# Performance work log

Hardware: AMD Instinct MI355X
Metric: run time of the kernel (lower is better)

## Reference

```python
import jax, jax.numpy as jnp
import numpy as np

N_NODES = 100000
D = 128            # node feature dim == hidden_units[0]
N_EDGES = 640000
BN_EPS = 1e-3      # keras BatchNormalization default epsilon


def setup_inputs() -> dict:
    key = jax.random.key(0)
    ks = jax.random.split(key, 12)
    node_repr = jax.random.normal(ks[0], (N_NODES, D), dtype=jnp.float32)
    edges = jax.random.randint(ks[1], (2, N_EDGES), 0, N_NODES, dtype=jnp.int64)
    # ffn_prepare: BN(D) -> Dense(D, gelu)   (dropout inactive at inference)
    bn1_gamma = jax.random.normal(ks[2], (D,), dtype=jnp.float32) * 0.1 + 1.0
    bn1_beta = jax.random.normal(ks[3], (D,), dtype=jnp.float32) * 0.1
    bn1_mean = jax.random.normal(ks[4], (D,), dtype=jnp.float32) * 0.1
    bn1_var = jax.random.uniform(ks[5], (D,), dtype=jnp.float32) + 0.5
    W1 = jax.random.normal(ks[6], (D, D), dtype=jnp.float32) / np.sqrt(D)
    b1 = jnp.zeros((D,), dtype=jnp.float32)
    # update_fn: BN(2D) -> Dense(D, gelu)
    bn2_gamma = jax.random.normal(ks[7], (2 * D,), dtype=jnp.float32) * 0.1 + 1.0
    bn2_beta = jax.random.normal(ks[8], (2 * D,), dtype=jnp.float32) * 0.1
    bn2_mean = jax.random.normal(ks[9], (2 * D,), dtype=jnp.float32) * 0.1
    bn2_var = jax.random.uniform(ks[10], (2 * D,), dtype=jnp.float32) + 0.5
    W2 = jax.random.normal(ks[11], (2 * D, D), dtype=jnp.float32) / np.sqrt(2 * D)
    b2 = jnp.zeros((D,), dtype=jnp.float32)
    return dict(node_repr=node_repr, edges=edges,
                bn1_gamma=bn1_gamma, bn1_beta=bn1_beta, bn1_mean=bn1_mean, bn1_var=bn1_var,
                W1=W1, b1=b1,
                bn2_gamma=bn2_gamma, bn2_beta=bn2_beta, bn2_mean=bn2_mean, bn2_var=bn2_var,
                W2=W2, b2=b2)


def _bn(x, gamma, beta, mean, var):
    # inference-mode batch norm
    return (x - mean) * jax.lax.rsqrt(var + BN_EPS) * gamma + beta


def reference(node_repr, edges, bn1_gamma, bn1_beta, bn1_mean, bn1_var, W1, b1,
              bn2_gamma, bn2_beta, bn2_mean, bn2_var, W2, b2):
    num_nodes = node_repr.shape[0]
    node_indices, neighbour_indices = edges[0], edges[1]
    # gather neighbour features: [E, D]
    neigh = node_repr[neighbour_indices]
    # prepare FFN (BN -> dropout(identity at eval) -> Dense + exact gelu)
    msg = jax.nn.gelu(_bn(neigh, bn1_gamma, bn1_beta, bn1_mean, bn1_var) @ W1 + b1,
                      approximate=False)
    # unsorted_segment_mean: sum / count, empty segments -> 0 (TF semantics)
    sums = jax.ops.segment_sum(msg, node_indices, num_segments=num_nodes)
    cnt = jax.ops.segment_sum(jnp.ones((edges.shape[1],), msg.dtype), node_indices,
                              num_segments=num_nodes)
    agg = sums / jnp.maximum(cnt, 1.0)[:, None]
    # update FFN on concat [node_repr, agg]: [N, 2D] -> [N, D]
    h = jnp.concatenate([node_repr, agg], axis=1)
    out = jax.nn.gelu(_bn(h, bn2_gamma, bn2_beta, bn2_mean, bn2_var) @ W2 + b2,
                      approximate=False)
    return out
```

## Files before the change

### kernel.cpp

```cpp
#include <hip/hip_runtime.h>

#define NN 100000
#define DD 128
#define EE 640000
#define BN_EPS 1e-3f
#define NBLK 391
#define NTILE 6250
#define EPB 1637
#define FFN1_BLKS 1563
#define FFN2_BLKS 768
#define LEMAX 4096

typedef __bf16 bf16x8 __attribute__((ext_vector_type(8)));
typedef float f32x4 __attribute__((ext_vector_type(4)));

#define W1F_OFF 0u
#define W2F_OFF 32768u
#define B1F_OFF 98304u
#define B2F_OFF 98816u
#define T_OFF   99328u
#define CNTG_OFF 25699328u
#define BOFS_OFF (25699328u + 611524u)
#define BSUM_OFF 26922376u
#define AGG_OFF  26926476u
#define AGG_OFF2 26926592u
#define XB_OFF   52526592u
#define PAIR_OFF 78126592u

__device__ __forceinline__ float gelu_fast(float x) {
    float x3 = x * x * x;
    float z2 = 1.5957691216057308f * x + 0.07135481627002407f * x3;
    return x / (1.0f + __expf(-z2));
}

__global__ __launch_bounds__(256) void prep_kernel(
    const float* __restrict__ g1, const float* __restrict__ be1,
    const float* __restrict__ m1, const float* __restrict__ v1,
    const float* __restrict__ W1, const float* __restrict__ b1,
    const float* __restrict__ g2, const float* __restrict__ be2,
    const float* __restrict__ m2, const float* __restrict__ v2,
    const float* __restrict__ W2, const float* __restrict__ b2,
    const int* __restrict__ edges,
    __bf16* __restrict__ W1f, __bf16* __restrict__ W2f,
    float* __restrict__ b1f, float* __restrict__ b2f,
    int* __restrict__ cntg)
{
    const int blk = blockIdx.x;
    const int t = threadIdx.x;
    if (blk < 64) {
        const int w = (blk * 256 + t) >> 6;
        const int lane = t & 63;
        if (w < 128) {
            float acc = 0.f;
            for (int k = lane; k < 128; k += 64) {
                float s = g1[k] * rsqrtf(v1[k] + BN_EPS);
                float sh = be1[k] - m1[k] * s;
                acc += sh * W1[k * 128 + w];
            }
#pragma unroll
            for (int off = 32; off > 0; off >>= 1) acc += __shfl_down(acc, off);
            if (lane == 0) b1f[w] = acc + b1[w];
        } else {
            const int n = w - 128;
            float acc = 0.f;
            for (int k = lane; k < 256; k += 64) {
                float s = g2[k] * rsqrtf(v2[k] + BN_EPS);
                float sh = be2[k] - m2[k] * s;
                acc += sh * W2[k * 128 + n];
            }
#pragma unroll
            for (int off = 32; off > 0; off >>= 1) acc += __shfl_down(acc, off);
            if (lane == 0) b2f[n] = acc + b2[n];
        }
    } else if (blk < 256) {
        int tid = (blk - 64) * 256 + t;
        if (tid < 16384) {
            int idx = tid;
            int i = idx & 7, l = (idx >> 3) & 63, nt = (idx >> 9) & 7, kt = idx >> 12;
            int k = kt * 32 + (l >> 4) * 8 + i;
            int n = nt * 16 + (l & 15);
            float s = g1[k] * rsqrtf(v1[k] + BN_EPS);
            W1f[idx] = (__bf16)(s * W1[k * 128 + n]);
        } else {
            int idx = tid - 16384;
            int i = idx & 7, l = (idx >> 3) & 63, nt = (idx >> 9) & 7, kt = idx >> 12;
            int n = nt * 16 + (l & 15);
            int row;
            if (kt < 4) {
                row = kt * 32 + (l >> 4) * 8 + i;
            } else {
                int q = (kt - 4) * 32 + (l >> 4) * 8 + i;
                row = 128 + ((q & 7) * 16 + (q >> 3));
            }
            float s = g2[row] * rsqrtf(v2[row] + BN_EPS);
            W2f[idx] = (__bf16)(s * W2[row * 128 + n]);
        }
    } else {
        __shared__ int cnt[NBLK];
        const int k = blk - 256;
        for (int b = t; b < NBLK; b += 256) cnt[b] = 0;
        __syncthreads();
        const int e0 = k * EPB, e1 = min(e0 + EPB, EE);
        for (int e = e0 + t; e < e1; e += 256)
            atomicAdd(&cnt[edges[e] >> 8], 1);
        __syncthreads();
        for (int b = t; b < NBLK; b += 256) cntg[k * NBLK + b] = cnt[b];
    }
}

__global__ __launch_bounds__(256) void sortb_kernel(const int* __restrict__ cntg,
                                                    int* __restrict__ bofs,
                                                    int* __restrict__ bsum)
{
    const int b = blockIdx.x, t = threadIdx.x;
    __shared__ int sp[256];
    int ia = 2 * t, ib = 2 * t + 1;
    int va = (ia < NBLK) ? cntg[ia * NBLK + b] : 0;
    int vb = (ib < NBLK) ? cntg[ib * NBLK + b] : 0;
    sp[t] = va + vb;
    __syncthreads();
    for (int off = 1; off < 256; off <<= 1) {
        int tmp = (t >= off) ? sp[t - off] : 0;
        __syncthreads();
        sp[t] += tmp;
        __syncthreads();
    }
    int pexcl = sp[t] - (va + vb);
    if (ia < NBLK) bofs[b * NBLK + ia] = pexcl;
    if (ib < NBLK) bofs[b * NBLK + ib] = pexcl + va;
    if (t == 255) bsum[b] = sp[255];
}

__global__ __launch_bounds__(256) void sortc_ffn1_kernel(
    const int* __restrict__ edges, const int* __restrict__ bsum,
    const int* __restrict__ bofs, int* __restrict__ pairbuf,
    const float* __restrict__ X, const __bf16* __restrict__ W1f,
    const float* __restrict__ b1f, __bf16* __restrict__ T,
    __bf16* __restrict__ Xb)
{
    __shared__ int sp[256];
    __shared__ int cur[NBLK];
    const int t = threadIdx.x;
    if (blockIdx.x < NBLK) {
        const int k = blockIdx.x;
        int ia = 2 * t, ib = 2 * t + 1;
        int va = (ia < NBLK) ? bsum[ia] : 0;
        int vb = (ib < NBLK) ? bsum[ib] : 0;
        sp[t] = va + vb;
        __syncthreads();
        for (int off = 1; off < 256; off <<= 1) {
            int tmp = (t >= off) ? sp[t - off] : 0;
            __syncthreads();
            sp[t] += tmp;
            __syncthreads();
        }
        int pexcl = sp[t] - (va + vb);
        if (ia < NBLK) cur[ia] = pexcl + bofs[ia * NBLK + k];
        if (ib < NBLK) cur[ib] = pexcl + va + bofs[ib * NBLK + k];
        __syncthreads();
        const int e0 = k * EPB, e1 = min(e0 + EPB, EE);
        for (int e = e0 + t; e < e1; e += 256) {
            int dst = edges[e];
            int src = edges[EE + e];
            int pos = atomicAdd(&cur[dst >> 8], 1);
            pairbuf[pos] = (src << 8) | (dst & 255);
        }
        return;
    }

    const int wave = t >> 6;
    const int lane = t & 63;
    const int tile = (blockIdx.x - NBLK) * 4 + wave;
    if (tile >= NTILE) return;
    const int c = lane & 15, kh = lane >> 4;

    const size_t rowb = (size_t)(tile * 16 + c) * DD;
    const float* xr = X + rowb + kh * 8;

    f32x4 r0[4], r1[4];
#pragma unroll
    for (int q = 0; q < 4; ++q) {
        r0[q] = *(const f32x4*)(xr + q * 32);
        r1[q] = *(const f32x4*)(xr + q * 32 + 4);
    }
    bf16x8 B[4][8];
#pragma unroll
    for (int kt = 0; kt < 4; ++kt)
#pragma unroll
        for (int nt = 0; nt < 8; ++nt)
            B[kt][nt] = *(const bf16x8*)(W1f + ((size_t)((kt * 8 + nt) * 64 + lane)) * 8);

    bf16x8 af[4];
#pragma unroll
    for (int kt = 0; kt < 4; ++kt) {
        bf16x8 fa;
#pragma unroll
        for (int i = 0; i < 4; ++i) { fa[i] = (__bf16)r0[kt][i]; fa[4 + i] = (__bf16)r1[kt][i]; }
        af[kt] = fa;
        *(bf16x8*)(Xb + rowb + kt * 32 + kh * 8) = fa;
    }

    f32x4 acc[8] = {};
#pragma unroll
    for (int kt = 0; kt < 4; ++kt)
#pragma unroll
        for (int nt = 0; nt < 8; ++nt)
            acc[nt] = __builtin_amdgcn_mfma_f32_16x16x32_bf16(af[kt], B[kt][nt], acc[nt], 0, 0, 0);

    float bias[8];
#pragma unroll
    for (int nt = 0; nt < 8; ++nt) bias[nt] = b1f[nt * 16 + c];

#pragma unroll
    for (int r = 0; r < 4; ++r) {
        int row = tile * 16 + kh * 4 + r;
        bf16x8 o;
#pragma unroll
        for (int nt = 0; nt < 8; ++nt)
            o[nt] = (__bf16)gelu_fast(acc[nt][r] + bias[nt]);
        *(bf16x8*)(T + (size_t)row * DD + c * 8) = o;
    }
}

__global__ __launch_bounds__(1024) void p2agg_kernel(
    const int* __restrict__ bsum, const int* __restrict__ pairbuf,
    const __bf16* __restrict__ T, __bf16* __restrict__ Agg)
{
    __shared__ int cnt[256];
    __shared__ int sArr[256];
    __shared__ int loff[257];
    __shared__ int red[16];
    __shared__ int lelist[LEMAX];
    const int b = blockIdx.x, t = threadIdx.x;
    const int lane = t & 63;

    int part = 0;
    for (int i = t; i < b; i += 1024) part += bsum[i];
#pragma unroll
    for (int off = 32; off > 0; off >>= 1) part += __shfl_down(part, off);
    if (lane == 0) red[t >> 6] = part;
    if (t < 256) cnt[t] = 0;
    __syncthreads();
    int start = 0;
#pragma unroll
    for (int i = 0; i < 16; ++i) start += red[i];
    const int tot = bsum[b];
    const int end = start + tot;

    for (int e = start + t; e < end; e += 1024)
        atomicAdd(&cnt[pairbuf[e] & 255], 1);
    __syncthreads();

    if (t < 256) sArr[t] = cnt[t];
    __syncthreads();
    for (int off = 1; off < 256; off <<= 1) {
        int tmp = (t < 256 && t >= off) ? sArr[t - off] : 0;
        __syncthreads();
        if (t < 256) sArr[t] += tmp;
        __syncthreads();
    }
    if (t < 256) {
        int ex = sArr[t] - cnt[t];
        loff[t] = ex;
        cnt[t] = ex;
    }
    if (t == 255) loff[256] = sArr[255];
    __syncthreads();

    for (int e = start + t; e < end; e += 1024) {
        int item = pairbuf[e];
        int pos = atomicAdd(&cnt[item & 255], 1);
        if (pos < LEMAX) lelist[pos] = item >> 8;
    }
    __syncthreads();

    const int j = t & 15;
    const int nl = t >> 4;
#pragma unroll
    for (int round = 0; round < 4; ++round) {
        const int nodeL = round * 64 + nl;
        const int node = b * 256 + nodeL;
        if (node >= NN) continue;
        const int lb = loff[nodeL], le = loff[nodeL + 1];
        float acc[8] = {};
        int e = lb;
        for (; e + 3 < le; e += 4) {
            int s0 = lelist[e], s1 = lelist[e + 1], s2 = lelist[e + 2], s3 = lelist[e + 3];
            bf16x8 v0 = *(const bf16x8*)(T + (size_t)s0 * DD + j * 8);
            bf16x8 v1 = *(const bf16x8*)(T + (size_t)s1 * DD + j * 8);
            bf16x8 v2 = *(const bf16x8*)(T + (size_t)s2 * DD + j * 8);
            bf16x8 v3 = *(const bf16x8*)(T + (size_t)s3 * DD + j * 8);
#pragma unroll
            for (int q = 0; q < 8; ++q)
                acc[q] += ((float)v0[q] + (float)v1[q]) + ((float)v2[q] + (float)v3[q]);
        }
        for (; e < le; ++e) {
            int s0 = lelist[e];
            bf16x8 v0 = *(const bf16x8*)(T + (size_t)s0 * DD + j * 8);
#pragma unroll
            for (int q = 0; q < 8; ++q) acc[q] += (float)v0[q];
        }
        const float inv = 1.0f / fmaxf((float)(le - lb), 1.0f);
        bf16x8 o;
#pragma unroll
        for (int q = 0; q < 8; ++q) o[q] = (__bf16)(acc[q] * inv);
        *(bf16x8*)(Agg + (size_t)node * DD + j * 8) = o;
    }
}

#define FFN2_LOAD(TT, XA, GA)                                              \
    {                                                                      \
        const size_t rb = (size_t)((TT) * 16 + c) * DD + kh * 8;           \
        _Pragma("unroll")                                                  \
        for (int q = 0; q < 4; ++q) {                                      \
            XA[q] = *(const bf16x8*)(Xb + rb + q * 32);                    \
            GA[q] = *(const bf16x8*)(Agg + rb + q * 32);                   \
        }                                                                  \
    }

#define FFN2_COMP(TT, XA, GA)                                              \
    {                                                                      \
        f32x4 acc0 = {}, acc1 = {};                                        \
        _Pragma("unroll")                                                  \
        for (int kt = 0; kt < 4; ++kt) {                                   \
            acc0 = __builtin_amdgcn_mfma_f32_16x16x32_bf16(XA[kt], Bf[kt][0], acc0, 0, 0, 0); \
            acc1 = __builtin_amdgcn_mfma_f32_16x16x32_bf16(XA[kt], Bf[kt][1], acc1, 0, 0, 0); \
        }                                                                  \
        _Pragma("unroll")                                                  \
        for (int kt = 0; kt < 4; ++kt) {                                   \
            acc0 = __builtin_amdgcn_mfma_f32_16x16x32_bf16(GA[kt], Bf[4 + kt][0], acc0, 0, 0, 0); \
            acc1 = __builtin_amdgcn_mfma_f32_16x16x32_bf16(GA[kt], Bf[4 + kt][1], acc1, 0, 0, 0); \
        }                                                                  \
        _Pragma("unroll")                                                  \
        for (int r = 0; r < 4; ++r) {                                      \
            int row = (TT) * 16 + kh * 4 + r;                              \
            out[(size_t)row * DD + (w * 2) * 16 + c] = gelu_fast(acc0[r] + bias0); \
            out[(size_t)row * DD + (w * 2 + 1) * 16 + c] = gelu_fast(acc1[r] + bias1); \
        }                                                                  \
    }

__global__ __launch_bounds__(256) void ffn2_kernel(
    const __bf16* __restrict__ Xb, const __bf16* __restrict__ Agg,
    const __bf16* __restrict__ W2f, const float* __restrict__ b2f,
    float* __restrict__ out)
{
    const int w = threadIdx.x >> 6;
    const int lane = threadIdx.x & 63;
    const int c = lane & 15, kh = lane >> 4;
    const int G = gridDim.x;

    bf16x8 Bf[8][2];
#pragma unroll
    for (int kt = 0; kt < 8; ++kt) {
        Bf[kt][0] = *(const bf16x8*)(W2f + ((size_t)((kt * 8 + w * 2) * 64 + lane)) * 8);
        Bf[kt][1] = *(const bf16x8*)(W2f + ((size_t)((kt * 8 + w * 2 + 1) * 64 + lane)) * 8);
    }
    const float bias0 = b2f[(w * 2) * 16 + c];
    const float bias1 = b2f[(w * 2 + 1) * 16 + c];

    int tile = blockIdx.x;
    if (tile >= NTILE) return;
    bf16x8 xa[4], ga[4], xb2[4], gb[4];
    FFN2_LOAD(tile, xa, ga);
    while (true) {
        int t2 = tile + G;
        if (t2 < NTILE) FFN2_LOAD(t2, xb2, gb);
        FFN2_COMP(tile, xa, ga);
        if (t2 >= NTILE) break;
        int t3 = t2 + G;
        if (t3 < NTILE) FFN2_LOAD(t3, xa, ga);
        FFN2_COMP(t2, xb2, gb);
        if (t3 >= NTILE) break;
        tile = t3;
    }
}

extern "C" void kernel_launch(void* const* d_in, const int* in_sizes, int n_in,
                              void* d_out, int out_size, void* d_ws, size_t ws_size,
                              hipStream_t stream) {
    const float* node_repr = (const float*)d_in[0];
    const int*   edges     = (const int*)d_in[1];
    const float* g1 = (const float*)d_in[2];
    const float* be1 = (const float*)d_in[3];
    const float* m1 = (const float*)d_in[4];
    const float* v1 = (const float*)d_in[5];
    const float* W1 = (const float*)d_in[6];
    const float* b1 = (const float*)d_in[7];
    const float* g2 = (const float*)d_in[8];
    const float* be2 = (const float*)d_in[9];
    const float* m2 = (const float*)d_in[10];
    const float* v2 = (const float*)d_in[11];
    const float* W2 = (const float*)d_in[12];
    const float* b2 = (const float*)d_in[13];

    char* ws = (char*)d_ws;
    __bf16* W1f = (__bf16*)(ws + W1F_OFF);
    __bf16* W2f = (__bf16*)(ws + W2F_OFF);
    float* b1f = (float*)(ws + B1F_OFF);
    float* b2f = (float*)(ws + B2F_OFF);
    __bf16* T  = (__bf16*)(ws + T_OFF);
    int* cntg  = (int*)(ws + CNTG_OFF);
    int* bofs  = (int*)(ws + BOFS_OFF);
    int* bsum  = (int*)(ws + BSUM_OFF);
    __bf16* Agg = (__bf16*)(ws + AGG_OFF2);
    __bf16* Xb  = (__bf16*)(ws + XB_OFF);
    int* pairbuf = (int*)(ws + PAIR_OFF);
    float* out = (float*)d_out;

    hipLaunchKernelGGL(prep_kernel, dim3(256 + NBLK), dim3(256), 0, stream,
                       g1, be1, m1, v1, W1, b1, g2, be2, m2, v2, W2, b2,
                       edges, W1f, W2f, b1f, b2f, cntg);

    hipLaunchKernelGGL(sortb_kernel, dim3(NBLK), dim3(256), 0, stream, cntg, bofs, bsum);

    hipLaunchKernelGGL(sortc_ffn1_kernel, dim3(NBLK + FFN1_BLKS), dim3(256), 0, stream,
                       edges, bsum, bofs, pairbuf, node_repr, W1f, b1f, T, Xb);

    hipLaunchKernelGGL(p2agg_kernel, dim3(NBLK), dim3(1024), 0, stream,
                       bsum, pairbuf, T, Agg);

    hipLaunchKernelGGL(ffn2_kernel, dim3(FFN2_BLKS), dim3(256), 0, stream,
                       Xb, Agg, W2f, b2f, out);
}
```

Baseline: 99.49 us.

## Fuse segment-mean aggregation with update FFN through shared-memory staging

Merges the aggregation kernel and the second FFN kernel into one. Each block now holds its 256 aggregated node rows in a swizzled 64KB LDS buffer that reuses the edge-list space, and then runs the MFMA update FFN directly on that buffer. This removes the global Agg write and read round trip and one kernel launch. In exchange, occupancy drops because of the large LDS footprint and 1024-thread blocks, the FFN2 stage no longer pipelines loads across tiles, and the grid is only 391 blocks.

```diff
diff --git a/kernel.cpp b/kernel.cpp
--- a/kernel.cpp
+++ b/kernel.cpp
@@ -8,7 +8,6 @@
 #define NTILE 6250
 #define EPB 1637
 #define FFN1_BLKS 1563
-#define FFN2_BLKS 768
 #define LEMAX 4096
 
 typedef __bf16 bf16x8 __attribute__((ext_vector_type(8)));
@@ -22,8 +21,6 @@
 #define CNTG_OFF 25699328u
 #define BOFS_OFF (25699328u + 611524u)
 #define BSUM_OFF 26922376u
-#define AGG_OFF  26926476u
-#define AGG_OFF2 26926592u
 #define XB_OFF   52526592u
 #define PAIR_OFF 78126592u
 
@@ -222,15 +219,20 @@
     }
 }
 
-__global__ __launch_bounds__(1024) void p2agg_kernel(
+__global__ __launch_bounds__(1024) void p2agg_ffn2_kernel(
     const int* __restrict__ bsum, const int* __restrict__ pairbuf,
-    const __bf16* __restrict__ T, __bf16* __restrict__ Agg)
+    const __bf16* __restrict__ T, const __bf16* __restrict__ Xb,
+    const __bf16* __restrict__ W2f, const float* __restrict__ b2f,
+    float* __restrict__ out)
 {
-    __shared__ int cnt[256];
-    __shared__ int sArr[256];
-    __shared__ int loff[257];
-    __shared__ int red[16];
-    __shared__ int lelist[LEMAX];
+    __shared__ char smem[65536];
+    int* lelist = (int*)smem;
+    int* cnt    = (int*)(smem + 16384);
+    int* sArr   = (int*)(smem + 17408);
+    int* loff   = (int*)(smem + 18432);
+    int* red    = (int*)(smem + 19460);
+    __bf16* aggL = (__bf16*)smem;
+
     const int b = blockIdx.x, t = threadIdx.x;
     const int lane = t & 63;
 
@@ -275,14 +277,17 @@
     __syncthreads();
 
     const int j = t & 15;
-    const int nl = t >> 4;
+    const int nl4 = t >> 4;
+    bf16x8 oreg[4];
+    int nlv[4];
 #pragma unroll
     for (int round = 0; round < 4; ++round) {
-        const int nodeL = round * 64 + nl;
+        const int nodeL = round * 64 + nl4;
+        nlv[round] = nodeL;
         const int node = b * 256 + nodeL;
-        if (node >= NN) continue;
-        const int lb = loff[nodeL], le = loff[nodeL + 1];
         float acc[8] = {};
+        int lb = 0, le = 0;
+        if (node < NN) { lb = loff[nodeL]; le = loff[nodeL + 1]; }
         int e = lb;
         for (; e + 3 < le; e += 4) {
             int s0 = lelist[e], s1 = lelist[e + 1], s2 = lelist[e + 2], s3 = lelist[e + 3];
@@ -304,74 +309,69 @@
         bf16x8 o;
 #pragma unroll
         for (int q = 0; q < 8; ++q) o[q] = (__bf16)(acc[q] * inv);
-        *(bf16x8*)(Agg + (size_t)node * DD + j * 8) = o;
-    }
-}
-
-#define FFN2_LOAD(TT, XA, GA)                                              \
-    {                                                                      \
-        const size_t rb = (size_t)((TT) * 16 + c) * DD + kh * 8;           \
-        _Pragma("unroll")                                                  \
-        for (int q = 0; q < 4; ++q) {                                      \
-            XA[q] = *(const bf16x8*)(Xb + rb + q * 32);                    \
-            GA[q] = *(const bf16x8*)(Agg + rb + q * 32);                   \
-        }                                                                  \
-    }
-
-#define FFN2_COMP(TT, XA, GA)                                              \
-    {                                                                      \
-        f32x4 acc0 = {}, acc1 = {};                                        \
-        _Pragma("unroll")                                                  \
-        for (int kt = 0; kt < 4; ++kt) {                                   \
-            acc0 = __builtin_amdgcn_mfma_f32_16x16x32_bf16(XA[kt], Bf[kt][0], acc0, 0, 0, 0); \
-            acc1 = __builtin_amdgcn_mfma_f32_16x16x32_bf16(XA[kt], Bf[kt][1], acc1, 0, 0, 0); \
-        }                                                                  \
-        _Pragma("unroll")                                                  \
-        for (int kt = 0; kt < 4; ++kt) {                                   \
-            acc0 = __builtin_amdgcn_mfma_f32_16x16x32_bf16(GA[kt], Bf[4 + kt][0], acc0, 0, 0, 0); \
-            acc1 = __builtin_amdgcn_mfma_f32_16x16x32_bf16(GA[kt], Bf[4 + kt][1], acc1, 0, 0, 0); \
-        }                                                                  \
-        _Pragma("unroll")                                                  \
-        for (int r = 0; r < 4; ++r) {                                      \
-            int row = (TT) * 16 + kh * 4 + r;                              \
-            out[(size_t)row * DD + (w * 2) * 16 + c] = gelu_fast(acc0[r] + bias0); \
-            out[(size_t)row * DD + (w * 2 + 1) * 16 + c] = gelu_fast(acc1[r] + bias1); \
-        }                                                                  \
-    }
-
-__global__ __launch_bounds__(256) void ffn2_kernel(
-    const __bf16* __restrict__ Xb, const __bf16* __restrict__ Agg,
-    const __bf16* __restrict__ W2f, const float* __restrict__ b2f,
-    float* __restrict__ out)
-{
-    const int w = threadIdx.x >> 6;
-    const int lane = threadIdx.x & 63;
+        oreg[round] = o;
+    }
+    __syncthreads();
+
+#pragma unroll
+    for (int round = 0; round < 4; ++round) {
+        int nl = nlv[round];
+        *(bf16x8*)(aggL + nl * 128 + ((j ^ (nl & 7)) * 8)) = oreg[round];
+    }
+    __syncthreads();
+
+    const int w4 = t >> 6;
+    const int q4 = w4 & 3;
+    const int tg = w4 >> 2;
     const int c = lane & 15, kh = lane >> 4;
-    const int G = gridDim.x;
 
     bf16x8 Bf[8][2];
 #pragma unroll
     for (int kt = 0; kt < 8; ++kt) {
-        Bf[kt][0] = *(const bf16x8*)(W2f + ((size_t)((kt * 8 + w * 2) * 64 + lane)) * 8);
-        Bf[kt][1] = *(const bf16x8*)(W2f + ((size_t)((kt * 8 + w * 2 + 1) * 64 + lane)) * 8);
-    }
-    const float bias0 = b2f[(w * 2) * 16 + c];
-    const float bias1 = b2f[(w * 2 + 1) * 16 + c];
-
-    int tile = blockIdx.x;
-    if (tile >= NTILE) return;
-    bf16x8 xa[4], ga[4], xb2[4], gb[4];
-    FFN2_LOAD(tile, xa, ga);
-    while (true) {
-        int t2 = tile + G;
-        if (t2 < NTILE) FFN2_LOAD(t2, xb2, gb);
-        FFN2_COMP(tile, xa, ga);
-        if (t2 >= NTILE) break;
-        int t3 = t2 + G;
-        if (t3 < NTILE) FFN2_LOAD(t3, xa, ga);
-        FFN2_COMP(t2, xb2, gb);
-        if (t3 >= NTILE) break;
-        tile = t3;
+        Bf[kt][0] = *(const bf16x8*)(W2f + ((size_t)((kt * 8 + q4 * 2) * 64 + lane)) * 8);
+        Bf[kt][1] = *(const bf16x8*)(W2f + ((size_t)((kt * 8 + q4 * 2 + 1) * 64 + lane)) * 8);
+    }
+    const float bias0 = b2f[(q4 * 2) * 16 + c];
+    const float bias1 = b2f[(q4 * 2 + 1) * 16 + c];
+
+#pragma unroll
+    for (int i = 0; i < 4; ++i) {
+        const int tl = tg * 4 + i;
+        const int rowbase = b * 256 + tl * 16;
+        if (rowbase >= NN) break;
+        int rA = rowbase + c; if (rA >= NN) rA = NN - 1;
+
+        bf16x8 xa[4], ga[4];
+        const size_t rb = (size_t)rA * DD + kh * 8;
+#pragma unroll
+        for (int kt = 0; kt < 4; ++kt)
+            xa[kt] = *(const bf16x8*)(Xb + rb + kt * 32);
+        const int lrow = tl * 16 + c;
+#pragma unroll
+        for (int kt = 0; kt < 4; ++kt) {
+            int slot = kt * 4 + kh;
+            ga[kt] = *(const bf16x8*)(aggL + lrow * 128 + ((slot ^ (lrow & 7)) * 8));
+        }
+
+        f32x4 acc0 = {}, acc1 = {};
+#pragma unroll
+        for (int kt = 0; kt < 4; ++kt) {
+            acc0 = __builtin_amdgcn_mfma_f32_16x16x32_bf16(xa[kt], Bf[kt][0], acc0, 0, 0, 0);
+            acc1 = __builtin_amdgcn_mfma_f32_16x16x32_bf16(xa[kt], Bf[kt][1], acc1, 0, 0, 0);
+        }
+#pragma unroll
+        for (int kt = 0; kt < 4; ++kt) {
+            acc0 = __builtin_amdgcn_mfma_f32_16x16x32_bf16(ga[kt], Bf[4 + kt][0], acc0, 0, 0, 0);
+            acc1 = __builtin_amdgcn_mfma_f32_16x16x32_bf16(ga[kt], Bf[4 + kt][1], acc1, 0, 0, 0);
+        }
+#pragma unroll
+        for (int r = 0; r < 4; ++r) {
+            int row = rowbase + kh * 4 + r;
+            if (row < NN) {
+                out[(size_t)row * DD + (q4 * 2) * 16 + c] = gelu_fast(acc0[r] + bias0);
+                out[(size_t)row * DD + (q4 * 2 + 1) * 16 + c] = gelu_fast(acc1[r] + bias1);
+            }
+        }
     }
 }
 
@@ -402,7 +402,6 @@
     int* cntg  = (int*)(ws + CNTG_OFF);
     int* bofs  = (int*)(ws + BOFS_OFF);
     int* bsum  = (int*)(ws + BSUM_OFF);
-    __bf16* Agg = (__bf16*)(ws + AGG_OFF2);
     __bf16* Xb  = (__bf16*)(ws + XB_OFF);
     int* pairbuf = (int*)(ws + PAIR_OFF);
     float* out = (float*)d_out;
@@ -416,9 +415,6 @@
     hipLaunchKernelGGL(sortc_ffn1_kernel, dim3(NBLK + FFN1_BLKS), dim3(256), 0, stream,
                        edges, bsum, bofs, pairbuf, node_repr, W1f, b1f, T, Xb);
 
-    hipLaunchKernelGGL(p2agg_kernel, dim3(NBLK), dim3(1024), 0, stream,
-                       bsum, pairbuf, T, Agg);
-
-    hipLaunchKernelGGL(ffn2_kernel, dim3(FFN2_BLKS), dim3(256), 0, stream,
-                       Xb, Agg, W2f, b2f, out);
-}
+    hipLaunchKernelGGL(p2agg_ffn2_kernel, dim3(NBLK), dim3(1024), 0, stream,
+                       bsum, pairbuf, T, Xb, W2f, b2f, out);
+}
```

Result: slower. 101.5 us (+2.1%).
